# Performance work log

Measured on AMD Instinct MI355X. Metric: run time of the kernel, lower is better.

Reference implementation:

```python
import jax, jax.numpy as jnp
import numpy as np

N_SRC = 50000
N_DST = 50000
E = 500000
H = 128
ED = 32
EPS = 1e-5


def _linear_params(key, fan_in, fan_out):
    kw, kb = jax.random.split(key)
    bound = 1.0 / np.sqrt(fan_in)
    W = jax.random.uniform(kw, (fan_in, fan_out), jnp.float32, -bound, bound)
    b = jax.random.uniform(kb, (fan_out,), jnp.float32, -bound, bound)
    return W, b


def setup_inputs() -> dict:
    key = jax.random.key(0)
    ks = jax.random.split(key, 12)
    src_x = jax.random.normal(ks[0], (N_SRC, H), jnp.float32)
    dst_x = jax.random.normal(ks[1], (N_DST, H), jnp.float32)
    edge_index = jax.random.randint(ks[2], (2, E), 0, N_DST, jnp.int64)
    edge_attr = jax.random.normal(ks[3], (E, ED), jnp.float32)
    Wsrc, bsrc = _linear_params(ks[4], H, H)
    Wdst, bdst = _linear_params(ks[5], H, H)
    We, be = _linear_params(ks[6], ED, H)
    Wattn, battn = _linear_params(ks[7], 3 * H, 1)
    Wmsg, bmsg = _linear_params(ks[8], H, H)
    Wout, bout = _linear_params(ks[9], 2 * H, H)
    gamma = jnp.ones((H,), jnp.float32)
    beta = jnp.zeros((H,), jnp.float32)
    return dict(src_x=src_x, dst_x=dst_x, edge_index=edge_index, edge_attr=edge_attr,
                Wsrc=Wsrc, bsrc=bsrc, Wdst=Wdst, bdst=bdst, We=We, be=be,
                Wattn=Wattn, battn=battn, Wmsg=Wmsg, bmsg=bmsg,
                Wout=Wout, bout=bout, gamma=gamma, beta=beta)


def _segment_softmax(scores, idx, num_segments):
    # numerically stable softmax over variable-size segments of dst index
    m = jax.ops.segment_max(scores, idx, num_segments=num_segments)
    ex = jnp.exp(scores - m[idx])
    s = jax.ops.segment_sum(ex, idx, num_segments=num_segments)
    return ex / s[idx]


def reference(src_x, dst_x, edge_index, edge_attr,
              Wsrc, bsrc, Wdst, bdst, We, be,
              Wattn, battn, Wmsg, bmsg, Wout, bout, gamma, beta):
    src_idx = edge_index[0]
    dst_idx = edge_index[1]
    num_dst = dst_x.shape[0]

    src_feat = src_x[src_idx] @ Wsrc + bsrc          # [E, H]
    dst_feat = dst_x[dst_idx] @ Wdst + bdst          # [E, H]
    e_feat = edge_attr @ We + be                     # [E, H]

    attn_in = jnp.concatenate([src_feat, dst_feat, e_feat], axis=-1)  # [E, 3H]
    msg = (src_feat + e_feat) @ Wmsg + bmsg          # [E, H]

    scores = (jnp.tanh(attn_in) @ Wattn + battn)[:, 0]  # [E]
    alpha = _segment_softmax(scores, dst_idx, num_dst)   # [E]

    agg = jax.ops.segment_sum(msg * alpha[:, None], dst_idx, num_segments=num_dst)  # [num_dst, H]

    updated = jnp.concatenate([dst_x, agg], axis=-1) @ Wout + bout
    # dropout is identity in eval mode
    h = dst_x + updated
    mu = jnp.mean(h, axis=-1, keepdims=True)
    var = jnp.var(h, axis=-1, keepdims=True)
    return (h - mu) * jax.lax.rsqrt(var + EPS) * gamma + beta
```

## Files before the change

kernel.cpp:

```cpp
#include <hip/hip_runtime.h>
#include <math.h>

#define NSRC 50000
#define NDST 50000
#define NE   500000
#define HD   128
#define EDIM 32
#define LN_EPS 1e-5f

typedef __attribute__((ext_vector_type(8))) short short8;
typedef __attribute__((ext_vector_type(4))) float f32x4;
typedef unsigned short u16;

#define TL2E 2.8853900817779268f
#define L2E  1.4426950408889634f

__device__ __forceinline__ float EXP2(float x) {
#if __has_builtin(__builtin_amdgcn_exp2f)
    return __builtin_amdgcn_exp2f(x);
#else
    return exp2f(x);
#endif
}
__device__ __forceinline__ float RCP(float x) {
#if __has_builtin(__builtin_amdgcn_rcpf)
    return __builtin_amdgcn_rcpf(x);
#else
    return 1.f / x;
#endif
}
__device__ __forceinline__ u16 f2b(float x) {
    unsigned u = __float_as_uint(x);
    return (u16)((u + 0x7FFFu + ((u >> 16) & 1u)) >> 16);
}
__device__ __forceinline__ float b2f(u16 h) {
    return __uint_as_float(((unsigned)h) << 16);
}
__device__ __forceinline__ short8 ld8(const u16* p) { return *(const short8*)p; }

__global__ __launch_bounds__(128) void fold1_kernel(
    const float* __restrict__ Wsrc, const float* __restrict__ bsrc,
    const float* __restrict__ We,   const float* __restrict__ be,
    const float* __restrict__ Wmsg, const float* __restrict__ bmsg,
    float* __restrict__ Wsm, float* __restrict__ bsm,
    float* __restrict__ WeMsg, float* __restrict__ c2,
    int* __restrict__ cnt)
{
    const int j = threadIdx.x;
    const int r = blockIdx.x;
    if (r >= 162) {
        int i = (r - 162) * 128 + j;
        if (i < NDST + 16) cnt[i] = 0;
        return;
    }
    float s = 0.f;
    if (r < 128) {
        for (int k = 0; k < 128; ++k) s += Wsrc[r*HD + k] * Wmsg[k*HD + j];
        Wsm[r*HD + j] = s;
    } else if (r < 160) {
        const int rr = r - 128;
        for (int k = 0; k < 128; ++k) s += We[rr*HD + k] * Wmsg[k*HD + j];
        WeMsg[rr*HD + j] = s;
    } else if (r == 160) {
        for (int k = 0; k < 128; ++k) s += bsrc[k] * Wmsg[k*HD + j];
        bsm[j] = s + bmsg[j];
    } else {
        for (int k = 0; k < 128; ++k) s += be[k] * Wmsg[k*HD + j];
        c2[j] = s;
    }
}

__global__ __launch_bounds__(64) void pack_all_kernel(
    const float* __restrict__ Wsrc, const float* __restrict__ Wdst,
    const float* __restrict__ Wsm,  const float* __restrict__ Wout,
    const float* __restrict__ We,   const float* __restrict__ WeMsg,
    const float* __restrict__ c2,   const float* __restrict__ bout,
    u16* __restrict__ Wsrc_pk, u16* __restrict__ Wdst_pk,
    u16* __restrict__ Wsm_pk,  u16* __restrict__ W1_pk,
    u16* __restrict__ W2_pk,   u16* __restrict__ We_pk,
    u16* __restrict__ W3_pk,   float* __restrict__ bias2)
{
    const int b = blockIdx.x;
    const int lane = threadIdx.x;
    const int ln = lane & 15, quad = lane >> 4;
    const float* Wout2 = Wout + HD*HD;

    if (b == 176) {
#pragma unroll
        for (int h = 0; h < 2; ++h) {
            const int col = lane + h*64;
            float s = 0.f;
            for (int k = 0; k < 128; ++k) s += c2[k] * Wout2[k*HD + col];
            bias2[col] = bout[col] + s;
        }
        return;
    }
    if (b >= 168) {
        const int t = b - 168;
        const int jj = t*16 + ln;
        float sacc[8] = {0,0,0,0,0,0,0,0};
        for (int k = 0; k < 128; ++k) {
            const float w2 = Wout2[k*HD + jj];
#pragma unroll
            for (int j = 0; j < 8; ++j)
                sacc[j] = fmaf(WeMsg[(quad*8 + j)*HD + k], w2, sacc[j]);
        }
        u16 tmp[8];
#pragma unroll
        for (int j = 0; j < 8; ++j) tmp[j] = f2b(sacc[j]);
        *(short8*)(W3_pk + (size_t)(t*64 + lane)*8) = *(short8*)tmp;
        return;
    }

    const float* src; u16* dst; int lb; float scl = 1.f; bool addI = false;
    if      (b < 32)  { src = Wsrc; dst = Wsrc_pk; lb = b;       scl = TL2E; }
    else if (b < 64)  { src = Wdst; dst = Wdst_pk; lb = b - 32;  scl = TL2E; }
    else if (b < 96)  { src = Wsm;  dst = Wsm_pk;  lb = b - 64; }
    else if (b < 128) { src = Wout; dst = W1_pk;   lb = b - 96;  addI = true; }
    else if (b < 160) { src = Wout2;dst = W2_pk;   lb = b - 128; }
    else              { src = We;   dst = We_pk;   lb = b - 160; scl = TL2E; }
    const int kc = lb >> 3, t = lb & 7;
    u16 tmp[8];
#pragma unroll
    for (int j = 0; j < 8; ++j) {
        const int i = kc*32 + quad*8 + j, jj = t*16 + ln;
        float v = src[(size_t)i*HD + jj] * scl;
        if (addI && i == jj) v += 1.f;
        tmp[j] = f2b(v);
    }
    *(short8*)(dst + (size_t)(lb*64 + lane)*8) = *(short8*)tmp;
}

#define NBLK 391
#define HB4 ((NE/4 + 255) / 256)

__global__ __launch_bounds__(256) void mega_kernel(
    const float* __restrict__ src_x, const float* __restrict__ dst_x,
    const int* __restrict__ ei,
    const u16* __restrict__ Wsrc_pk, const u16* __restrict__ Wsm_pk,
    const u16* __restrict__ Wdst_pk,
    const float* __restrict__ bsrc, const float* __restrict__ bsm,
    const float* __restrict__ bdst, const float* __restrict__ wattn,
    float* __restrict__ s1, float* __restrict__ s2,
    u16* __restrict__ srcmsgb, int* __restrict__ cnt, int* __restrict__ rank)
{
    __shared__ __align__(16) u16 wlds[16384];
    __shared__ __align__(16) u16 tlds[4][2048];
    const int t = threadIdx.x;
    const int blk = blockIdx.x;

    if (blk >= 2*NBLK) {
        const int idx = (blk - 2*NBLK) * 256 + t;
        if (idx < NE/4) {
            int4 d4 = ((const int4*)(ei + NE))[idx];
            int4 r4;
            r4.x = atomicAdd(&cnt[d4.x], 1);
            r4.y = atomicAdd(&cnt[d4.y], 1);
            r4.z = atomicAdd(&cnt[d4.z], 1);
            r4.w = atomicAdd(&cnt[d4.w], 1);
            ((int4*)rank)[idx] = r4;
        }
        return;
    }

    const int w = t >> 6, lane = t & 63;
    const int ln = lane & 15, quad = lane >> 4;
    const bool is_src = (blk < NBLK);
    const int b = is_src ? blk : blk - NBLK;
    int row0 = b * 128 + w * 32;
    if (row0 > NSRC - 32) row0 = NSRC - 32;

    const float* X = is_src ? src_x : dst_x;
    const float* rp0 = X + (size_t)(row0 + ln)*HD;
    const float* rp1 = rp0 + (size_t)16*HD;
    short8 a0[4], a1[4];
#pragma unroll
    for (int kc = 0; kc < 4; ++kc) {
        float4 f0 = *(const float4*)(rp0 + kc*32 + quad*8);
        float4 f1 = *(const float4*)(rp0 + kc*32 + quad*8 + 4);
        float4 g0 = *(const float4*)(rp1 + kc*32 + quad*8);
        float4 g1 = *(const float4*)(rp1 + kc*32 + quad*8 + 4);
        u16 tb[8] = { f2b(f0.x), f2b(f0.y), f2b(f0.z), f2b(f0.w),
                      f2b(f1.x), f2b(f1.y), f2b(f1.z), f2b(f1.w) };
        a0[kc] = *(short8*)tb;
        u16 tc[8] = { f2b(g0.x), f2b(g0.y), f2b(g0.z), f2b(g0.w),
                      f2b(g1.x), f2b(g1.y), f2b(g1.z), f2b(g1.w) };
        a1[kc] = *(short8*)tc;
    }

    const u16* Wpk = is_src ? Wsrc_pk : Wdst_pk;
#pragma unroll
    for (int it = 0; it < 8; ++it) {
        short8 v = ld8(Wpk + (size_t)(it*256 + t)*8);
        *(short8*)(&wlds[(it*256 + t)*8]) = v;
    }
    __syncthreads();

    const float* bb_ = is_src ? bsrc : bdst;
    const float* wa  = is_src ? wattn : wattn + HD;
    float* sout      = is_src ? s1 : s2;

    float v0[4] = {0,0,0,0}, v1[4] = {0,0,0,0};
    float ws = 0.f;
#pragma unroll
    for (int tt = 0; tt < 8; ++tt) {
        const float bb = bb_[tt*16 + ln] * TL2E;
        const float ww = wa[tt*16 + ln];
        f32x4 acc0 = {bb, bb, bb, bb};
        f32x4 acc1 = {bb, bb, bb, bb};
#pragma unroll
        for (int kc = 0; kc < 4; ++kc) {
            short8 bf = ld8(&wlds[(size_t)((kc*8 + tt)*64 + lane)*8]);
            acc0 = __builtin_amdgcn_mfma_f32_16x16x32_bf16(a0[kc], bf, acc0, 0, 0, 0);
            acc1 = __builtin_amdgcn_mfma_f32_16x16x32_bf16(a1[kc], bf, acc1, 0, 0, 0);
        }
        ws += ww;
#pragma unroll
        for (int r = 0; r < 4; ++r) {
            v0[r] = fmaf(ww, RCP(EXP2(acc0[r]) + 1.f), v0[r]);
            v1[r] = fmaf(ww, RCP(EXP2(acc1[r]) + 1.f), v1[r]);
        }
    }
#pragma unroll
    for (int off = 8; off >= 1; off >>= 1) {
        ws += __shfl_xor(ws, off);
#pragma unroll
        for (int r = 0; r < 4; ++r) {
            v0[r] += __shfl_xor(v0[r], off);
            v1[r] += __shfl_xor(v1[r], off);
        }
    }
    if (ln == 0) {
#pragma unroll
        for (int r = 0; r < 4; ++r) {
            sout[row0 + quad*4 + r]      = fmaf(-2.f, v0[r], ws);
            sout[row0 + 16 + quad*4 + r] = fmaf(-2.f, v1[r], ws);
        }
    }

    if (!is_src) return;

    __syncthreads();
#pragma unroll
    for (int it = 0; it < 8; ++it) {
        short8 v = ld8(Wsm_pk + (size_t)(it*256 + t)*8);
        *(short8*)(&wlds[(it*256 + t)*8]) = v;
    }
    __syncthreads();

    u16* slab = &tlds[w][0];
#pragma unroll
    for (int tile = 0; tile < 2; ++tile) {
#pragma unroll
        for (int tt = 0; tt < 8; ++tt) {
            const float bs = bsm[tt*16 + ln];
            f32x4 acc = {bs, bs, bs, bs};
#pragma unroll
            for (int kc = 0; kc < 4; ++kc) {
                short8 bf = ld8(&wlds[(size_t)((kc*8 + tt)*64 + lane)*8]);
                acc = __builtin_amdgcn_mfma_f32_16x16x32_bf16(
                          tile ? a1[kc] : a0[kc], bf, acc, 0, 0, 0);
            }
#pragma unroll
            for (int r = 0; r < 4; ++r)
                slab[(quad*4 + r)*128 + ((tt ^ quad) << 4) + ln] = f2b(acc[r]);
        }
#pragma unroll
        for (int r2 = 0; r2 < 4; ++r2) {
            const int row = r2*4 + quad;
            const int c = ln*8;
            const int sidx = row*128 + (((c >> 4) ^ r2) << 4) + (c & 15);
            short8 val = *(const short8*)(&slab[sidx]);
            *(short8*)(srcmsgb + (size_t)(row0 + tile*16 + row)*HD + c) = val;
        }
    }
}

__global__ __launch_bounds__(1024) void scan1_kernel(
    const int* __restrict__ cnt, int* __restrict__ excl, int* __restrict__ bsum)
{
    __shared__ int buf[1024];
    const int t = threadIdx.x;
    const int i = blockIdx.x * 1024 + t;
    int v = (i < NDST) ? cnt[i] : 0;
    buf[t] = v;
    __syncthreads();
    for (int off = 1; off < 1024; off <<= 1) {
        int tv = (t >= off) ? buf[t - off] : 0;
        __syncthreads();
        buf[t] += tv;
        __syncthreads();
    }
    if (i < NDST) excl[i] = buf[t] - v;
    if (t == 1023) bsum[blockIdx.x] = buf[1023];
}

__global__ __launch_bounds__(256) void scan23_kernel(
    const int* __restrict__ bsum, int* __restrict__ rowptr)
{
    __shared__ int pref[64];
    const int t = threadIdx.x;
    const int NB = (NDST + 1023) / 1024;
    if (t < 64) {
        int orig = (t < NB) ? bsum[t] : 0;
        int v = orig;
        for (int off = 1; off < 64; off <<= 1) {
            int u = __shfl_up(v, off);
            if (t >= off) v += u;
        }
        pref[t] = v - orig;
        if (blockIdx.x == 0 && t == NB - 1) rowptr[NDST] = v;
    }
    __syncthreads();
    const int i = blockIdx.x * 256 + t;
    if (i < NDST) rowptr[i] += pref[i >> 10];
}

__global__ __launch_bounds__(256) void edge_score_kernel(
    const int* __restrict__ ei, const float* __restrict__ eattr,
    const u16* __restrict__ We_pk, const float* __restrict__ be,
    const float* __restrict__ wattn, const float* __restrict__ battn,
    const float* __restrict__ s1, const float* __restrict__ s2,
    const int* __restrict__ rowptr, const int* __restrict__ rank,
    int4* __restrict__ ev16)
{
    const int t = threadIdx.x;
    const int w = t >> 6, lane = t & 63;
    const int ln = lane & 15, quad = lane >> 4;
    const int e0 = (blockIdx.x * 4 + w) * 16;
    if (e0 >= NE) return;

    const float* ap = eattr + (size_t)(e0 + ln)*EDIM + quad*8;
    float4 f0 = *(const float4*)(ap);
    float4 f1 = *(const float4*)(ap + 4);
    u16 ab[8] = { f2b(f0.x), f2b(f0.y), f2b(f0.z), f2b(f0.w),
                  f2b(f1.x), f2b(f1.y), f2b(f1.z), f2b(f1.w) };
    short8 a = *(short8*)ab;

    const float* wa3 = wattn + 2*HD;
    float v[4] = {0.f, 0.f, 0.f, 0.f};
    float ws = 0.f;
#pragma unroll
    for (int tt = 0; tt < 8; ++tt) {
        const float bb = be[tt*16 + ln] * TL2E;
        const float ww = wa3[tt*16 + ln];
        f32x4 acc = {bb, bb, bb, bb};
        short8 b = ld8(We_pk + (size_t)(tt*64 + lane)*8);
        acc = __builtin_amdgcn_mfma_f32_16x16x32_bf16(a, b, acc, 0, 0, 0);
        ws += ww;
#pragma unroll
        for (int r = 0; r < 4; ++r)
            v[r] = fmaf(ww, RCP(EXP2(acc[r]) + 1.f), v[r]);
    }
#pragma unroll
    for (int off = 8; off >= 1; off >>= 1) {
        ws += __shfl_xor(ws, off);
#pragma unroll
        for (int r = 0; r < 4; ++r) v[r] += __shfl_xor(v[r], off);
    }
    const int srcq = (ln >> 2) << 4;
    float sv0 = __shfl(v[0], srcq);
    float sv1 = __shfl(v[1], srcq);
    float sv2 = __shfl(v[2], srcq);
    float sv3 = __shfl(v[3], srcq);
    const int rr = ln & 3;
    float vlo = (rr & 1) ? sv1 : sv0;
    float vhi = (rr & 1) ? sv3 : sv2;
    float vv  = (rr & 2) ? vhi : vlo;

    if (quad == 0) {
        const int e = e0 + ln;
        const int srcn = ei[e];
        const int dstn = ei[NE + e];
        float sc = (fmaf(-2.f, vv, ws) + s1[srcn] + s2[dstn] + battn[0]) * L2E;
        const int pos = rowptr[dstn] + rank[e];
        ev16[pos] = make_int4(srcn, e, __float_as_int(sc), 0);
    }
}

__global__ __launch_bounds__(256) void dst_agg_kernel(
    const int4* __restrict__ ev16, const int* __restrict__ rowptr,
    const u16* __restrict__ srcmsgb, const float* __restrict__ eattr,
    const float* __restrict__ c2,
    u16* __restrict__ aggSb, u16* __restrict__ weab)
{
    const int lane = threadIdx.x & 63;
    const int d = blockIdx.x * 4 + (threadIdx.x >> 6);
    const int el = lane >> 4, c = lane & 15;
    const int start = rowptr[d], end = rowptr[d + 1];

    if (start == end) {
        if (el == 0) {
            u16 z[8];
#pragma unroll
            for (int j = 0; j < 8; ++j) z[j] = f2b(-c2[c*8 + j]);
            *(short8*)(aggSb + (size_t)d*HD + c*8) = *(short8*)z;
            if (c < 8) {
                u16 zz[4] = {0,0,0,0};
                *(ushort4*)(weab + (size_t)d*EDIM + c*4) = *(ushort4*)zz;
            }
        }
        return;
    }

    float sacc = 0.f;
    float acc[8]  = {0,0,0,0,0,0,0,0};
    float wacc[4] = {0,0,0,0};

    int icur = start + el;
    bool vcur = (icur < end);
    int iicur = vcur ? icur : start;
    int4 q = ev16[iicur];

    for (int i0 = start; i0 < end; i0 += 4) {
        const float wgt = vcur ? EXP2(__int_as_float(q.z)) : 0.f;
        const int   srow = q.x;
        const int   ecur = q.y;
        const int inx = i0 + 4 + el;
        vcur = (inx < end);
        iicur = vcur ? inx : start;
        q = ev16[iicur];

        sacc += wgt;
        short8 sm = ld8(srcmsgb + (size_t)srow*HD + c*8);
#pragma unroll
        for (int j = 0; j < 8; ++j)
            acc[j] = fmaf(wgt, b2f(((u16*)&sm)[j]), acc[j]);
        if (c < 8) {
            float4 f = *(const float4*)(eattr + (size_t)ecur*EDIM + c*4);
            wacc[0] = fmaf(wgt, f.x, wacc[0]);
            wacc[1] = fmaf(wgt, f.y, wacc[1]);
            wacc[2] = fmaf(wgt, f.z, wacc[2]);
            wacc[3] = fmaf(wgt, f.w, wacc[3]);
        }
    }
#pragma unroll
    for (int off = 16; off <= 32; off <<= 1) {
        sacc += __shfl_xor(sacc, off);
#pragma unroll
        for (int j = 0; j < 8; ++j) acc[j] += __shfl_xor(acc[j], off);
#pragma unroll
        for (int j = 0; j < 4; ++j) wacc[j] += __shfl_xor(wacc[j], off);
    }
    const float inv = RCP(sacc);
    if (el == 0) {
        u16 o[8];
#pragma unroll
        for (int j = 0; j < 8; ++j) o[j] = f2b(acc[j] * inv);
        *(short8*)(aggSb + (size_t)d*HD + c*8) = *(short8*)o;
        if (c < 8) {
            u16 o2[4];
#pragma unroll
            for (int j = 0; j < 4; ++j) o2[j] = f2b(wacc[j] * inv);
            *(ushort4*)(weab + (size_t)d*EDIM + c*4) = *(ushort4*)o2;
        }
    }
}

__global__ __launch_bounds__(256) void final_kernel(
    const float* __restrict__ dst_x, const u16* __restrict__ aggSb,
    const u16* __restrict__ weab,
    const u16* __restrict__ W1_pk, const u16* __restrict__ W2_pk,
    const u16* __restrict__ W3_pk, const float* __restrict__ bias2,
    const float* __restrict__ gamma, const float* __restrict__ beta,
    float* __restrict__ out)
{
    const int t = threadIdx.x;
    const int w = t >> 6, lane = t & 63;
    const int ln = lane & 15, quad = lane >> 4;
    int row0 = (blockIdx.x * 4 + w) * 16;
    if (row0 > NDST - 16) row0 = NDST - 16;

    const float* rp = dst_x + (size_t)(row0 + ln)*HD;
    short8 a1[4], a2[4], a3;
#pragma unroll
    for (int kc = 0; kc < 4; ++kc) {
        float4 f0 = *(const float4*)(rp + kc*32 + quad*8);
        float4 f1 = *(const float4*)(rp + kc*32 + quad*8 + 4);
        u16 tb[8] = { f2b(f0.x), f2b(f0.y), f2b(f0.z), f2b(f0.w),
                      f2b(f1.x), f2b(f1.y), f2b(f1.z), f2b(f1.w) };
        a1[kc] = *(short8*)tb;
        a2[kc] = ld8(aggSb + (size_t)(row0 + ln)*HD + kc*32 + quad*8);
    }
    a3 = ld8(weab + (size_t)(row0 + ln)*EDIM + quad*8);

    f32x4 accs[8];
#pragma unroll
    for (int tt = 0; tt < 8; ++tt) {
        const float bb = bias2[tt*16 + ln];
        f32x4 acc = {bb, bb, bb, bb};
#pragma unroll
        for (int kc = 0; kc < 4; ++kc) {
            short8 b = ld8(W1_pk + (size_t)((kc*8 + tt)*64 + lane)*8);
            acc = __builtin_amdgcn_mfma_f32_16x16x32_bf16(a1[kc], b, acc, 0, 0, 0);
        }
#pragma unroll
        for (int kc = 0; kc < 4; ++kc) {
            short8 b = ld8(W2_pk + (size_t)((kc*8 + tt)*64 + lane)*8);
            acc = __builtin_amdgcn_mfma_f32_16x16x32_bf16(a2[kc], b, acc, 0, 0, 0);
        }
        {
            short8 b = ld8(W3_pk + (size_t)(tt*64 + lane)*8);
            acc = __builtin_amdgcn_mfma_f32_16x16x32_bf16(a3, b, acc, 0, 0, 0);
        }
        accs[tt] = acc;
    }

    const float gl[8] = { gamma[ln], gamma[16+ln], gamma[32+ln], gamma[48+ln],
                          gamma[64+ln], gamma[80+ln], gamma[96+ln], gamma[112+ln] };
    const float bl[8] = { beta[ln], beta[16+ln], beta[32+ln], beta[48+ln],
                          beta[64+ln], beta[80+ln], beta[96+ln], beta[112+ln] };
#pragma unroll
    for (int r = 0; r < 4; ++r) {
        float s = 0.f, qq = 0.f;
#pragma unroll
        for (int tt = 0; tt < 8; ++tt) {
            float u = accs[tt][r];
            s += u; qq += u*u;
        }
#pragma unroll
        for (int off = 8; off >= 1; off >>= 1) {
            s  += __shfl_xor(s, off);
            qq += __shfl_xor(qq, off);
        }
        const float mean = s * (1.f / HD);
        const float var  = qq * (1.f / HD) - mean * mean;
        const float rstd = rsqrtf(var + LN_EPS);
        const int row = row0 + quad*4 + r;
#pragma unroll
        for (int tt = 0; tt < 8; ++tt)
            out[(size_t)row*HD + tt*16 + ln] =
                (accs[tt][r] - mean) * rstd * gl[tt] + bl[tt];
    }
}

extern "C" void kernel_launch(void* const* d_in, const int* in_sizes, int n_in,
                              void* d_out, int out_size, void* d_ws, size_t ws_size,
                              hipStream_t stream)
{
    const float* src_x = (const float*)d_in[0];
    const float* dst_x = (const float*)d_in[1];
    const int*   ei    = (const int*)d_in[2];
    const float* eattr = (const float*)d_in[3];
    const float* Wsrc  = (const float*)d_in[4];
    const float* bsrc  = (const float*)d_in[5];
    const float* Wdst  = (const float*)d_in[6];
    const float* bdst  = (const float*)d_in[7];
    const float* We    = (const float*)d_in[8];
    const float* be    = (const float*)d_in[9];
    const float* Wattn = (const float*)d_in[10];
    const float* battn = (const float*)d_in[11];
    const float* Wmsg  = (const float*)d_in[12];
    const float* bmsg  = (const float*)d_in[13];
    const float* Wout  = (const float*)d_in[14];
    const float* bout  = (const float*)d_in[15];
    const float* gamma = (const float*)d_in[16];
    const float* beta  = (const float*)d_in[17];
    float* out = (float*)d_out;

    float* ws = (float*)d_ws;
    u16* srcmsgb = (u16*)(ws + 0);
    u16* aggSb   = (u16*)(ws + 3200000);
    u16* weab    = (u16*)(ws + 6400000);
    float* s1    = ws + 7200000;
    float* s2    = ws + 7250048;
    float* Wsm   = ws + 7300096;
    float* bsm   = ws + 7316480;
    float* WeMsg = ws + 7316608;
    float* c2    = ws + 7320704;
    float* bias2 = ws + 7320832;
    u16* Wsrc_pk = (u16*)(ws + 7320960);
    u16* Wdst_pk = (u16*)(ws + 7329152);
    u16* Wsm_pk  = (u16*)(ws + 7337344);
    u16* W1_pk   = (u16*)(ws + 7345536);
    u16* W2_pk   = (u16*)(ws + 7353728);
    u16* We_pk   = (u16*)(ws + 7361920);
    u16* W3_pk   = (u16*)(ws + 7363968);
    int* rowptr  = (int*)(ws + 7366016);
    int* cnt     = (int*)(ws + 7416032);
    int* bsum    = (int*)(ws + 7466048);
    int* rank    = (int*)(ws + 7466112);
    int4* ev16   = (int4*)(ws + 7966112);

    fold1_kernel<<<553, 128, 0, stream>>>(Wsrc, bsrc, We, be, Wmsg, bmsg,
                                          Wsm, bsm, WeMsg, c2, cnt);
    pack_all_kernel<<<177, 64, 0, stream>>>(Wsrc, Wdst, Wsm, Wout, We, WeMsg,
                                            c2, bout,
                                            Wsrc_pk, Wdst_pk, Wsm_pk, W1_pk,
                                            W2_pk, We_pk, W3_pk, bias2);

    mega_kernel<<<2*NBLK + HB4, 256, 0, stream>>>(
        src_x, dst_x, ei, Wsrc_pk, Wsm_pk, Wdst_pk,
        bsrc, bsm, bdst, Wattn, s1, s2, srcmsgb, cnt, rank);

    scan1_kernel<<<(NDST + 1023) / 1024, 1024, 0, stream>>>(cnt, rowptr, bsum);
    scan23_kernel<<<(NDST + 255) / 256, 256, 0, stream>>>(bsum, rowptr);

    edge_score_kernel<<<(NE/16 + 3) / 4, 256, 0, stream>>>(
        ei, eattr, We_pk, be, Wattn, battn, s1, s2, rowptr, rank, ev16);

    dst_agg_kernel<<<NDST / 4, 256, 0, stream>>>(ev16, rowptr, srcmsgb,
                                                 eattr, c2, aggSb, weab);

    final_kernel<<<(NDST/16 + 3) / 4, 256, 0, stream>>>(
        dst_x, aggSb, weab, W1_pk, W2_pk, W3_pk, bias2, gamma, beta, out);
}
```

Baseline: 303.2 us.

## Precompute scaled attention constants and process 64 edges per wave in edge scoring

A new pack block precomputes the attention weights pre-scaled by -2*log2(e), the biases pre-scaled, and the constant sums, so the mega and edge-score kernels drop their per-thread weight-sum reductions and final scaling. The edge-score kernel now handles 64 edges per wave, four MFMA tiles sharing each We fragment load, and every lane writes one edge instead of only a quarter of the lanes. The last wave clamps its start to NE-64, so some edges are recomputed and written twice with identical values. This trades more registers per wave for fewer weight loads and better lane utilisation.

```diff
diff --git a/kernel.cpp b/kernel.cpp
--- a/kernel.cpp
+++ b/kernel.cpp
@@ -75,16 +75,50 @@
     const float* __restrict__ Wsm,  const float* __restrict__ Wout,
     const float* __restrict__ We,   const float* __restrict__ WeMsg,
     const float* __restrict__ c2,   const float* __restrict__ bout,
+    const float* __restrict__ bsrc, const float* __restrict__ bdst,
+    const float* __restrict__ be,   const float* __restrict__ battn,
+    const float* __restrict__ wattn,
     u16* __restrict__ Wsrc_pk, u16* __restrict__ Wdst_pk,
     u16* __restrict__ Wsm_pk,  u16* __restrict__ W1_pk,
     u16* __restrict__ W2_pk,   u16* __restrict__ We_pk,
-    u16* __restrict__ W3_pk,   float* __restrict__ bias2)
+    u16* __restrict__ W3_pk,   float* __restrict__ bias2,
+    float* __restrict__ wa1s, float* __restrict__ wa2s,
+    float* __restrict__ wa3s, float* __restrict__ bsrcs,
+    float* __restrict__ bdsts, float* __restrict__ bes,
+    float* __restrict__ consts)
 {
     const int b = blockIdx.x;
     const int lane = threadIdx.x;
     const int ln = lane & 15, quad = lane >> 4;
     const float* Wout2 = Wout + HD*HD;
 
+    if (b == 177) {
+        float sa1 = 0.f, sa2 = 0.f, sa3 = 0.f;
+#pragma unroll
+        for (int h = 0; h < 2; ++h) {
+            const int col = lane + h*64;
+            float a1 = wattn[col], a2 = wattn[HD + col], a3 = wattn[2*HD + col];
+            wa1s[col] = a1 * (-2.f * L2E);
+            wa2s[col] = a2 * (-2.f * L2E);
+            wa3s[col] = a3 * (-2.f * L2E);
+            bsrcs[col] = bsrc[col] * TL2E;
+            bdsts[col] = bdst[col] * TL2E;
+            bes[col]   = be[col]   * TL2E;
+            sa1 += a1; sa2 += a2; sa3 += a3;
+        }
+#pragma unroll
+        for (int off = 32; off >= 1; off >>= 1) {
+            sa1 += __shfl_xor(sa1, off);
+            sa2 += __shfl_xor(sa2, off);
+            sa3 += __shfl_xor(sa3, off);
+        }
+        if (lane == 0) {
+            consts[0] = L2E * sa1;
+            consts[1] = L2E * sa2;
+            consts[2] = L2E * (sa3 + battn[0]);
+        }
+        return;
+    }
     if (b == 176) {
 #pragma unroll
         for (int h = 0; h < 2; ++h) {
@@ -139,8 +173,10 @@
     const int* __restrict__ ei,
     const u16* __restrict__ Wsrc_pk, const u16* __restrict__ Wsm_pk,
     const u16* __restrict__ Wdst_pk,
-    const float* __restrict__ bsrc, const float* __restrict__ bsm,
-    const float* __restrict__ bdst, const float* __restrict__ wattn,
+    const float* __restrict__ bsrcs, const float* __restrict__ bsm,
+    const float* __restrict__ bdsts,
+    const float* __restrict__ wa1s, const float* __restrict__ wa2s,
+    const float* __restrict__ consts,
     float* __restrict__ s1, float* __restrict__ s2,
     u16* __restrict__ srcmsgb, int* __restrict__ cnt, int* __restrict__ rank)
 {
@@ -196,15 +232,15 @@
     }
     __syncthreads();
 
-    const float* bb_ = is_src ? bsrc : bdst;
-    const float* wa  = is_src ? wattn : wattn + HD;
+    const float* bb_ = is_src ? bsrcs : bdsts;
+    const float* wa  = is_src ? wa1s : wa2s;
+    const float  K   = consts[is_src ? 0 : 1];
     float* sout      = is_src ? s1 : s2;
 
     float v0[4] = {0,0,0,0}, v1[4] = {0,0,0,0};
-    float ws = 0.f;
 #pragma unroll
     for (int tt = 0; tt < 8; ++tt) {
-        const float bb = bb_[tt*16 + ln] * TL2E;
+        const float bb = bb_[tt*16 + ln];
         const float ww = wa[tt*16 + ln];
         f32x4 acc0 = {bb, bb, bb, bb};
         f32x4 acc1 = {bb, bb, bb, bb};
@@ -214,7 +250,6 @@
             acc0 = __builtin_amdgcn_mfma_f32_16x16x32_bf16(a0[kc], bf, acc0, 0, 0, 0);
             acc1 = __builtin_amdgcn_mfma_f32_16x16x32_bf16(a1[kc], bf, acc1, 0, 0, 0);
         }
-        ws += ww;
 #pragma unroll
         for (int r = 0; r < 4; ++r) {
             v0[r] = fmaf(ww, RCP(EXP2(acc0[r]) + 1.f), v0[r]);
@@ -223,7 +258,6 @@
     }
 #pragma unroll
     for (int off = 8; off >= 1; off >>= 1) {
-        ws += __shfl_xor(ws, off);
 #pragma unroll
         for (int r = 0; r < 4; ++r) {
             v0[r] += __shfl_xor(v0[r], off);
@@ -233,8 +267,8 @@
     if (ln == 0) {
 #pragma unroll
         for (int r = 0; r < 4; ++r) {
-            sout[row0 + quad*4 + r]      = fmaf(-2.f, v0[r], ws);
-            sout[row0 + 16 + quad*4 + r] = fmaf(-2.f, v1[r], ws);
+            sout[row0 + quad*4 + r]      = K + v0[r];
+            sout[row0 + 16 + quad*4 + r] = K + v1[r];
         }
     }
 
@@ -318,8 +352,8 @@
 
 __global__ __launch_bounds__(256) void edge_score_kernel(
     const int* __restrict__ ei, const float* __restrict__ eattr,
-    const u16* __restrict__ We_pk, const float* __restrict__ be,
-    const float* __restrict__ wattn, const float* __restrict__ battn,
+    const u16* __restrict__ We_pk, const float* __restrict__ bes,
+    const float* __restrict__ wa3s, const float* __restrict__ consts,
     const float* __restrict__ s1, const float* __restrict__ s2,
     const int* __restrict__ rowptr, const int* __restrict__ rank,
     int4* __restrict__ ev16)
@@ -327,55 +361,78 @@
     const int t = threadIdx.x;
     const int w = t >> 6, lane = t & 63;
     const int ln = lane & 15, quad = lane >> 4;
-    const int e0 = (blockIdx.x * 4 + w) * 16;
-    if (e0 >= NE) return;
-
-    const float* ap = eattr + (size_t)(e0 + ln)*EDIM + quad*8;
-    float4 f0 = *(const float4*)(ap);
-    float4 f1 = *(const float4*)(ap + 4);
-    u16 ab[8] = { f2b(f0.x), f2b(f0.y), f2b(f0.z), f2b(f0.w),
-                  f2b(f1.x), f2b(f1.y), f2b(f1.z), f2b(f1.w) };
-    short8 a = *(short8*)ab;
-
-    const float* wa3 = wattn + 2*HD;
-    float v[4] = {0.f, 0.f, 0.f, 0.f};
-    float ws = 0.f;
+    int e0 = (blockIdx.x * 4 + w) * 64;
+    if (e0 > NE - 64) e0 = NE - 64;
+
+    short8 a[4];
+#pragma unroll
+    for (int tl = 0; tl < 4; ++tl) {
+        const float* ap = eattr + (size_t)(e0 + tl*16 + ln)*EDIM + quad*8;
+        float4 f0 = *(const float4*)(ap);
+        float4 f1 = *(const float4*)(ap + 4);
+        u16 ab[8] = { f2b(f0.x), f2b(f0.y), f2b(f0.z), f2b(f0.w),
+                      f2b(f1.x), f2b(f1.y), f2b(f1.z), f2b(f1.w) };
+        a[tl] = *(short8*)ab;
+    }
+
+    float v0[4] = {0,0,0,0}, v1[4] = {0,0,0,0};
+    float v2[4] = {0,0,0,0}, v3[4] = {0,0,0,0};
 #pragma unroll
     for (int tt = 0; tt < 8; ++tt) {
-        const float bb = be[tt*16 + ln] * TL2E;
-        const float ww = wa3[tt*16 + ln];
-        f32x4 acc = {bb, bb, bb, bb};
+        const float bb = bes[tt*16 + ln];
+        const float ww = wa3s[tt*16 + ln];
         short8 b = ld8(We_pk + (size_t)(tt*64 + lane)*8);
-        acc = __builtin_amdgcn_mfma_f32_16x16x32_bf16(a, b, acc, 0, 0, 0);
-        ws += ww;
-#pragma unroll
-        for (int r = 0; r < 4; ++r)
-            v[r] = fmaf(ww, RCP(EXP2(acc[r]) + 1.f), v[r]);
+        f32x4 ac0 = {bb, bb, bb, bb};
+        f32x4 ac1 = {bb, bb, bb, bb};
+        f32x4 ac2 = {bb, bb, bb, bb};
+        f32x4 ac3 = {bb, bb, bb, bb};
+        ac0 = __builtin_amdgcn_mfma_f32_16x16x32_bf16(a[0], b, ac0, 0, 0, 0);
+        ac1 = __builtin_amdgcn_mfma_f32_16x16x32_bf16(a[1], b, ac1, 0, 0, 0);
+        ac2 = __builtin_amdgcn_mfma_f32_16x16x32_bf16(a[2], b, ac2, 0, 0, 0);
+        ac3 = __builtin_amdgcn_mfma_f32_16x16x32_bf16(a[3], b, ac3, 0, 0, 0);
+#pragma unroll
+        for (int r = 0; r < 4; ++r) {
+            v0[r] = fmaf(ww, RCP(EXP2(ac0[r]) + 1.f), v0[r]);
+            v1[r] = fmaf(ww, RCP(EXP2(ac1[r]) + 1.f), v1[r]);
+            v2[r] = fmaf(ww, RCP(EXP2(ac2[r]) + 1.f), v2[r]);
+            v3[r] = fmaf(ww, RCP(EXP2(ac3[r]) + 1.f), v3[r]);
+        }
     }
 #pragma unroll
     for (int off = 8; off >= 1; off >>= 1) {
-        ws += __shfl_xor(ws, off);
-#pragma unroll
-        for (int r = 0; r < 4; ++r) v[r] += __shfl_xor(v[r], off);
-    }
-    const int srcq = (ln >> 2) << 4;
-    float sv0 = __shfl(v[0], srcq);
-    float sv1 = __shfl(v[1], srcq);
-    float sv2 = __shfl(v[2], srcq);
-    float sv3 = __shfl(v[3], srcq);
-    const int rr = ln & 3;
-    float vlo = (rr & 1) ? sv1 : sv0;
-    float vhi = (rr & 1) ? sv3 : sv2;
-    float vv  = (rr & 2) ? vhi : vlo;
-
-    if (quad == 0) {
-        const int e = e0 + ln;
-        const int srcn = ei[e];
-        const int dstn = ei[NE + e];
-        float sc = (fmaf(-2.f, vv, ws) + s1[srcn] + s2[dstn] + battn[0]) * L2E;
-        const int pos = rowptr[dstn] + rank[e];
-        ev16[pos] = make_int4(srcn, e, __float_as_int(sc), 0);
-    }
+#pragma unroll
+        for (int r = 0; r < 4; ++r) {
+            v0[r] += __shfl_xor(v0[r], off);
+            v1[r] += __shfl_xor(v1[r], off);
+            v2[r] += __shfl_xor(v2[r], off);
+            v3[r] += __shfl_xor(v3[r], off);
+        }
+    }
+    const bool s0 = ln & 1, s1b = ln & 2, s2b = ln & 4, s3b = ln & 8;
+    float m00 = s0 ? v0[1] : v0[0];
+    float m01 = s0 ? v0[3] : v0[2];
+    float m02 = s0 ? v1[1] : v1[0];
+    float m03 = s0 ? v1[3] : v1[2];
+    float m04 = s0 ? v2[1] : v2[0];
+    float m05 = s0 ? v2[3] : v2[2];
+    float m06 = s0 ? v3[1] : v3[0];
+    float m07 = s0 ? v3[3] : v3[2];
+    float m10 = s1b ? m01 : m00;
+    float m11 = s1b ? m03 : m02;
+    float m12 = s1b ? m05 : m04;
+    float m13 = s1b ? m07 : m06;
+    float m20 = s2b ? m11 : m10;
+    float m21 = s2b ? m13 : m12;
+    float selv = s3b ? m21 : m20;
+    const int srcl = ((lane >> 2) & 3) * 16 + ((lane >> 4) << 2) + (lane & 3);
+    const float myv = __shfl(selv, srcl);
+
+    const int e = e0 + lane;
+    const int srcn = ei[e];
+    const int dstn = ei[NE + e];
+    const float sc = consts[2] + s1[srcn] + s2[dstn] + myv;
+    const int pos = rowptr[dstn] + rank[e];
+    ev16[pos] = make_int4(srcn, e, __float_as_int(sc), 0);
 }
 
 __global__ __launch_bounds__(256) void dst_agg_kernel(
@@ -581,23 +638,33 @@
     int* bsum    = (int*)(ws + 7466048);
     int* rank    = (int*)(ws + 7466112);
     int4* ev16   = (int4*)(ws + 7966112);
+    float* wa1s  = ws + 9966112;
+    float* wa2s  = ws + 9966240;
+    float* wa3s  = ws + 9966368;
+    float* bsrcs = ws + 9966496;
+    float* bdsts = ws + 9966624;
+    float* bes   = ws + 9966752;
+    float* consts= ws + 9966880;
 
     fold1_kernel<<<553, 128, 0, stream>>>(Wsrc, bsrc, We, be, Wmsg, bmsg,
                                           Wsm, bsm, WeMsg, c2, cnt);
-    pack_all_kernel<<<177, 64, 0, stream>>>(Wsrc, Wdst, Wsm, Wout, We, WeMsg,
-                                            c2, bout,
+    pack_all_kernel<<<178, 64, 0, stream>>>(Wsrc, Wdst, Wsm, Wout, We, WeMsg,
+                                            c2, bout, bsrc, bdst, be, battn,
+                                            Wattn,
                                             Wsrc_pk, Wdst_pk, Wsm_pk, W1_pk,
-                                            W2_pk, We_pk, W3_pk, bias2);
+                                            W2_pk, We_pk, W3_pk, bias2,
+                                            wa1s, wa2s, wa3s, bsrcs, bdsts,
+                                            bes, consts);
 
     mega_kernel<<<2*NBLK + HB4, 256, 0, stream>>>(
         src_x, dst_x, ei, Wsrc_pk, Wsm_pk, Wdst_pk,
-        bsrc, bsm, bdst, Wattn, s1, s2, srcmsgb, cnt, rank);
+        bsrcs, bsm, bdsts, wa1s, wa2s, consts, s1, s2, srcmsgb, cnt, rank);
 
     scan1_kernel<<<(NDST + 1023) / 1024, 1024, 0, stream>>>(cnt, rowptr, bsum);
     scan23_kernel<<<(NDST + 255) / 256, 256, 0, stream>>>(bsum, rowptr);
 
-    edge_score_kernel<<<(NE/16 + 3) / 4, 256, 0, stream>>>(
-        ei, eattr, We_pk, be, Wattn, battn, s1, s2, rowptr, rank, ev16);
+    edge_score_kernel<<<((NE + 63)/64 + 3) / 4, 256, 0, stream>>>(
+        ei, eattr, We_pk, bes, wa3s, consts, s1, s2, rowptr, rank, ev16);
 
     dst_agg_kernel<<<NDST / 4, 256, 0, stream>>>(ev16, rowptr, srcmsgb,
                                                  eattr, c2, aggSb, weab);
```

Measured after the change: 295.7 us. -2.5%, faster.
